# Kernel tuning notes

Measured on AMD Instinct MI355X. Metric: run time of the kernel, lower is better.

The kernel has to match this reference:

```python
import jax, jax.numpy as jnp
import numpy as np

TOP_K = 2


def setup_inputs() -> dict:
    key = jax.random.key(0)
    k1, k2, k3, k4, k5 = jax.random.split(key, 5)
    H, F, E = 1024, 2048, 8
    B, S = 2, 1024
    return {
        "hidden_states": jax.random.normal(k1, (B, S, H), dtype=jnp.float32),
        "gate_w": jax.random.normal(k2, (E, H), dtype=jnp.float32) * (1.0 / np.sqrt(H)),
        "w1": jax.random.normal(k3, (E, F, H), dtype=jnp.float32) * (1.0 / np.sqrt(H)),
        "w2": jax.random.normal(k4, (E, H, F), dtype=jnp.float32) * (1.0 / np.sqrt(F)),
        "w3": jax.random.normal(k5, (E, F, H), dtype=jnp.float32) * (1.0 / np.sqrt(H)),
    }


def reference(hidden_states, gate_w, w1, w2, w3):
    B, S, H = hidden_states.shape
    E = gate_w.shape[0]
    x = hidden_states.reshape(-1, H)  # [T, H]

    # Router: softmax in float32, top-k, renormalize (exact Mixtral math)
    router_logits = x @ gate_w.T  # [T, E]
    probs = jax.nn.softmax(router_logits.astype(jnp.float32), axis=-1)
    routing_weights, selected = jax.lax.top_k(probs, TOP_K)  # [T, K]
    routing_weights = routing_weights / routing_weights.sum(axis=-1, keepdims=True)
    routing_weights = routing_weights.astype(x.dtype)

    # Per-token combine weight for each expert: [T, E]
    combine = (jax.nn.one_hot(selected, E, dtype=x.dtype) * routing_weights[..., None]).sum(axis=1)

    # Dense grouped expert SwiGLU MLP (zero combine weight for unselected experts
    # makes this strictly equivalent to the gathered/dispatched computation)
    h = jnp.einsum('th,efh->etf', x, w1)   # [E, T, F]
    g = jnp.einsum('th,efh->etf', x, w3)   # [E, T, F]
    mid = jax.nn.silu(h) * g               # SwiGLU
    expert_out = jnp.einsum('etf,ehf->eth', mid, w2)  # [E, T, H]
    out = jnp.einsum('eth,te->th', expert_out, combine)  # weighted combine

    return out.reshape(B, S, H), router_logits
```

## Files before the change

### kernel.cpp

```cpp
#include <hip/hip_runtime.h>
#include <hip/hip_bf16.h>
#include <math.h>

#define H 1024
#define FF 2048
#define E 8
#define T 2048
#define NSLOT (2*T)
#define SLOT_PAD 128

typedef __attribute__((ext_vector_type(8))) short s16x8;
typedef __attribute__((ext_vector_type(4))) float f32x4;

static __device__ __forceinline__ unsigned short f2bf(float f) {
    union { float f; unsigned u; } v; v.f = f;
    unsigned r = v.u + 0x7fff + ((v.u >> 16) & 1);
    return (unsigned short)(r >> 16);
}

__global__ __launch_bounds__(256) void router_kernel(
    const float* __restrict__ x, const float* __restrict__ gw,
    float* __restrict__ logits_out, int* __restrict__ top_id,
    float* __restrict__ top_w, int* __restrict__ counts)
{
    int t = blockIdx.x;
    int tid = threadIdx.x;
    int e = tid >> 5;
    int l32 = tid & 31;
    const float* xr = x + (size_t)t * H;
    const float* gr = gw + (size_t)e * H;
    float s = 0.f;
    for (int h = l32; h < H; h += 32) s += xr[h] * gr[h];
    for (int off = 16; off; off >>= 1) s += __shfl_down(s, off, 32);
    __shared__ float lg[E];
    if (l32 == 0) lg[e] = s;
    __syncthreads();
    if (tid < E) logits_out[(size_t)t * E + tid] = lg[tid];
    if (tid == 0) {
        int i1 = 0; float b1 = lg[0];
        for (int i = 1; i < E; ++i) if (lg[i] > b1) { b1 = lg[i]; i1 = i; }
        int i2 = -1; float b2 = -INFINITY;
        for (int i = 0; i < E; ++i) if (i != i1 && lg[i] > b2) { b2 = lg[i]; i2 = i; }
        float p2 = expf(b2 - b1);
        float inv = 1.f / (1.f + p2);
        top_id[2*t]   = i1;  top_id[2*t+1] = i2;
        top_w[2*t]    = inv; top_w[2*t+1]  = p2 * inv;
        atomicAdd(&counts[i1], 1);
        atomicAdd(&counts[i2], 1);
    }
}

__global__ void scan_kernel(const int* __restrict__ counts,
                            int* __restrict__ offsets, int* __restrict__ cursors)
{
    if (threadIdx.x == 0) {
        int acc = 0;
        for (int i = 0; i < E; ++i) { offsets[i] = acc; acc += counts[i]; }
        offsets[E] = acc;
    }
    if (threadIdx.x < E) cursors[threadIdx.x] = 0;
}

__global__ __launch_bounds__(256) void assign_kernel(
    const float* __restrict__ x, const int* __restrict__ top_id,
    const float* __restrict__ top_w, const int* __restrict__ offsets,
    int* __restrict__ cursors, int* __restrict__ slot_token,
    float* __restrict__ slot_w, unsigned short* __restrict__ xg)
{
    int t = blockIdx.x, tid = threadIdx.x;
    __shared__ int pos[2];
    if (tid == 0) {
        for (int k = 0; k < 2; ++k) {
            int e = top_id[2*t + k];
            int p = offsets[e] + atomicAdd(&cursors[e], 1);
            slot_token[p] = t;
            slot_w[p] = top_w[2*t + k];
            pos[k] = p;
        }
    }
    __syncthreads();
    float4 xv = ((const float4*)(x + (size_t)t * H))[tid];
    ushort4 b;
    b.x = f2bf(xv.x); b.y = f2bf(xv.y); b.z = f2bf(xv.z); b.w = f2bf(xv.w);
    ((ushort4*)(xg + (size_t)pos[0] * H))[tid] = b;
    ((ushort4*)(xg + (size_t)pos[1] * H))[tid] = b;
}

__global__ __launch_bounds__(256) void gemm1_kernel(
    const unsigned short* __restrict__ xg,
    const float* __restrict__ w1, const float* __restrict__ w3,
    const int* __restrict__ offsets, unsigned short* __restrict__ mid)
{
    int e = blockIdx.z;
    int off = offsets[e];
    int cnt = offsets[e + 1] - off;
    int m0 = blockIdx.y * 128;
    if (m0 >= cnt) return;
    int f0 = blockIdx.x * 64;

    __shared__ __align__(16) unsigned short sx[128][72];
    __shared__ __align__(16) unsigned short s1[64][72];
    __shared__ __align__(16) unsigned short s3[64][72];

    int tid = threadIdx.x;
    int wave = tid >> 6, lane = tid & 63;
    int quad = lane >> 4, l16 = lane & 15;
    int wm = wave & 1, wn = wave >> 1;

    f32x4 acc1[4][2] = {{{0.f,0.f,0.f,0.f}}};
    f32x4 acc3[4][2] = {{{0.f,0.f,0.f,0.f}}};

    int sxr = tid >> 3, sxc = (tid & 7) * 8;
    int swr = tid >> 2, swc = (tid & 3) * 16;

    const unsigned short* xgp = xg + (size_t)(off + m0 + sxr) * H + sxc;
    const float* w1p = w1 + ((size_t)e * FF + f0 + swr) * H + swc;
    const float* w3p = w3 + ((size_t)e * FF + f0 + swr) * H + swc;

    for (int k0 = 0; k0 < H; k0 += 64) {
        #pragma unroll
        for (int rr = 0; rr < 128; rr += 32) {
            uint4 v = *(const uint4*)(xgp + (size_t)rr * H + k0);
            *(uint4*)&sx[sxr + rr][sxc] = v;
        }
        #pragma unroll
        for (int c = 0; c < 16; c += 4) {
            float4 a1 = *(const float4*)(w1p + k0 + c);
            float4 a3 = *(const float4*)(w3p + k0 + c);
            ushort4 c1, c3;
            c1.x = f2bf(a1.x); c1.y = f2bf(a1.y); c1.z = f2bf(a1.z); c1.w = f2bf(a1.w);
            c3.x = f2bf(a3.x); c3.y = f2bf(a3.y); c3.z = f2bf(a3.z); c3.w = f2bf(a3.w);
            *(ushort4*)&s1[swr][swc + c] = c1;
            *(ushort4*)&s3[swr][swc + c] = c3;
        }
        __syncthreads();
        #pragma unroll
        for (int ks = 0; ks < 2; ++ks) {
            int kk = ks * 32 + quad * 8;
            s16x8 a[4], b1[2], b3[2];
            #pragma unroll
            for (int i = 0; i < 4; ++i)
                a[i] = *(const s16x8*)&sx[wm * 64 + i * 16 + l16][kk];
            #pragma unroll
            for (int j = 0; j < 2; ++j) {
                b1[j] = *(const s16x8*)&s1[wn * 32 + j * 16 + l16][kk];
                b3[j] = *(const s16x8*)&s3[wn * 32 + j * 16 + l16][kk];
            }
            #pragma unroll
            for (int i = 0; i < 4; ++i)
                #pragma unroll
                for (int j = 0; j < 2; ++j) {
                    acc1[i][j] = __builtin_amdgcn_mfma_f32_16x16x32_bf16(a[i], b1[j], acc1[i][j], 0, 0, 0);
                    acc3[i][j] = __builtin_amdgcn_mfma_f32_16x16x32_bf16(a[i], b3[j], acc3[i][j], 0, 0, 0);
                }
        }
        __syncthreads();
    }

    #pragma unroll
    for (int i = 0; i < 4; ++i) {
        #pragma unroll
        for (int r = 0; r < 4; ++r) {
            int row = wm * 64 + i * 16 + quad * 4 + r;
            if (m0 + row < cnt) {
                size_t base = (size_t)(off + m0 + row) * FF + f0 + wn * 32;
                #pragma unroll
                for (int j = 0; j < 2; ++j) {
                    float h = acc1[i][j][r];
                    float g = acc3[i][j][r];
                    float v = h / (1.f + __expf(-h)) * g;
                    mid[base + j * 16 + l16] = f2bf(v);
                }
            }
        }
    }
}

__global__ __launch_bounds__(256) void gemm2_kernel(
    const unsigned short* __restrict__ mid, const float* __restrict__ w2,
    const int* __restrict__ offsets, const int* __restrict__ slot_token,
    const float* __restrict__ slot_w, float* __restrict__ out)
{
    int e = blockIdx.z;
    int off = offsets[e];
    int cnt = offsets[e + 1] - off;
    int m0 = blockIdx.y * 128;
    if (m0 >= cnt) return;
    int n0 = blockIdx.x * 64;

    __shared__ __align__(16) unsigned short sa[128][72];
    __shared__ __align__(16) unsigned short sb[64][72];

    int tid = threadIdx.x;
    int wave = tid >> 6, lane = tid & 63;
    int quad = lane >> 4, l16 = lane & 15;
    int wm = wave & 1, wn = wave >> 1;

    f32x4 acc[4][2] = {{{0.f,0.f,0.f,0.f}}};

    int sxr = tid >> 3, sxc = (tid & 7) * 8;
    int swr = tid >> 2, swc = (tid & 3) * 16;

    const unsigned short* ap = mid + (size_t)(off + m0 + sxr) * FF + sxc;
    const float* bp = w2 + ((size_t)e * H + n0 + swr) * FF + swc;

    for (int k0 = 0; k0 < FF; k0 += 64) {
        #pragma unroll
        for (int rr = 0; rr < 128; rr += 32) {
            uint4 v = *(const uint4*)(ap + (size_t)rr * FF + k0);
            *(uint4*)&sa[sxr + rr][sxc] = v;
        }
        #pragma unroll
        for (int c = 0; c < 16; c += 4) {
            float4 a = *(const float4*)(bp + k0 + c);
            ushort4 cb;
            cb.x = f2bf(a.x); cb.y = f2bf(a.y); cb.z = f2bf(a.z); cb.w = f2bf(a.w);
            *(ushort4*)&sb[swr][swc + c] = cb;
        }
        __syncthreads();
        #pragma unroll
        for (int ks = 0; ks < 2; ++ks) {
            int kk = ks * 32 + quad * 8;
            s16x8 a[4], b[2];
            #pragma unroll
            for (int i = 0; i < 4; ++i)
                a[i] = *(const s16x8*)&sa[wm * 64 + i * 16 + l16][kk];
            #pragma unroll
            for (int j = 0; j < 2; ++j)
                b[j] = *(const s16x8*)&sb[wn * 32 + j * 16 + l16][kk];
            #pragma unroll
            for (int i = 0; i < 4; ++i)
                #pragma unroll
                for (int j = 0; j < 2; ++j)
                    acc[i][j] = __builtin_amdgcn_mfma_f32_16x16x32_bf16(a[i], b[j], acc[i][j], 0, 0, 0);
        }
        __syncthreads();
    }

    #pragma unroll
    for (int i = 0; i < 4; ++i) {
        #pragma unroll
        for (int r = 0; r < 4; ++r) {
            int row = wm * 64 + i * 16 + quad * 4 + r;
            if (m0 + row < cnt) {
                int slot = off + m0 + row;
                int tok = slot_token[slot];
                float wgt = slot_w[slot];
                float* orow = out + (size_t)tok * H + n0 + wn * 32;
                #pragma unroll
                for (int j = 0; j < 2; ++j)
                    atomicAdd(&orow[j * 16 + l16], acc[i][j][r] * wgt);
            }
        }
    }
}

extern "C" void kernel_launch(void* const* d_in, const int* in_sizes, int n_in,
                              void* d_out, int out_size, void* d_ws, size_t ws_size,
                              hipStream_t stream) {
    const float* x  = (const float*)d_in[0];
    const float* gw = (const float*)d_in[1];
    const float* w1 = (const float*)d_in[2];
    const float* w2 = (const float*)d_in[3];
    const float* w3 = (const float*)d_in[4];
    float* out    = (float*)d_out;
    float* logits = out + (size_t)T * H;

    int* counts       = (int*)d_ws;
    int* cursors      = counts + 8;
    int* offsets      = cursors + 8;
    int* top_id       = counts + 64;
    float* top_w      = (float*)(top_id + 2*T);
    int* slot_token   = (int*)(top_w + 2*T);
    float* slot_w     = (float*)(slot_token + NSLOT);
    unsigned short* xg  = (unsigned short*)(slot_w + NSLOT);
    unsigned short* mid = xg + (size_t)(NSLOT + SLOT_PAD) * H;

    hipMemsetAsync(counts, 0, 64 * sizeof(int), stream);
    hipMemsetAsync(out, 0, (size_t)T * H * sizeof(float), stream);

    router_kernel<<<T, 256, 0, stream>>>(x, gw, logits, top_id, top_w, counts);
    scan_kernel<<<1, 64, 0, stream>>>(counts, offsets, cursors);
    assign_kernel<<<T, 256, 0, stream>>>(x, top_id, top_w, offsets, cursors,
                                         slot_token, slot_w, xg);
    gemm1_kernel<<<dim3(FF / 64, 16, E), 256, 0, stream>>>(xg, w1, w3, offsets, mid);
    gemm2_kernel<<<dim3(H / 64, 16, E), 256, 0, stream>>>(mid, w2, offsets,
                                                          slot_token, slot_w, out);
}
```

Baseline: 462.5 us.

## Pre-convert expert weights to bf16, use direct global-to-LDS loads, replace atomics with combine

```diff
diff --git a/kernel.cpp b/kernel.cpp
--- a/kernel.cpp
+++ b/kernel.cpp
@@ -16,6 +16,36 @@
     union { float f; unsigned u; } v; v.f = f;
     unsigned r = v.u + 0x7fff + ((v.u >> 16) & 1);
     return (unsigned short)(r >> 16);
+}
+static __device__ __forceinline__ float bf2f(unsigned short s) {
+    union { unsigned u; float f; } v; v.u = ((unsigned)s) << 16;
+    return v.f;
+}
+
+typedef __attribute__((address_space(3))) unsigned int lds_uint;
+typedef const __attribute__((address_space(1))) unsigned int glob_uint;
+static __device__ __forceinline__ void gl_lds16(const void* g, void* l) {
+    __builtin_amdgcn_global_load_lds((glob_uint*)g, (lds_uint*)l, 16, 0, 0);
+}
+
+__global__ __launch_bounds__(256) void convert_kernel(
+    const float* __restrict__ w1, const float* __restrict__ w3,
+    const float* __restrict__ w2, unsigned short* __restrict__ w1b,
+    unsigned short* __restrict__ w3b, unsigned short* __restrict__ w2b)
+{
+    const float* s; unsigned short* d;
+    if (blockIdx.y == 0)      { s = w1; d = w1b; }
+    else if (blockIdx.y == 1) { s = w3; d = w3b; }
+    else                      { s = w2; d = w2b; }
+    size_t i = ((size_t)blockIdx.x * 256 + threadIdx.x) * 8;
+    float4 a = *(const float4*)(s + i);
+    float4 b = *(const float4*)(s + i + 4);
+    uint4 st;
+    st.x = f2bf(a.x) | ((unsigned)f2bf(a.y) << 16);
+    st.y = f2bf(a.z) | ((unsigned)f2bf(a.w) << 16);
+    st.z = f2bf(b.x) | ((unsigned)f2bf(b.y) << 16);
+    st.w = f2bf(b.z) | ((unsigned)f2bf(b.w) << 16);
+    *(uint4*)(d + i) = st;
 }
 
 __global__ __launch_bounds__(256) void router_kernel(
@@ -63,9 +93,8 @@
 
 __global__ __launch_bounds__(256) void assign_kernel(
     const float* __restrict__ x, const int* __restrict__ top_id,
-    const float* __restrict__ top_w, const int* __restrict__ offsets,
-    int* __restrict__ cursors, int* __restrict__ slot_token,
-    float* __restrict__ slot_w, unsigned short* __restrict__ xg)
+    const int* __restrict__ offsets, int* __restrict__ cursors,
+    int* __restrict__ top_pos, unsigned short* __restrict__ xg)
 {
     int t = blockIdx.x, tid = threadIdx.x;
     __shared__ int pos[2];
@@ -73,8 +102,7 @@
         for (int k = 0; k < 2; ++k) {
             int e = top_id[2*t + k];
             int p = offsets[e] + atomicAdd(&cursors[e], 1);
-            slot_token[p] = t;
-            slot_w[p] = top_w[2*t + k];
+            top_pos[2*t + k] = p;
             pos[k] = p;
         }
     }
@@ -88,7 +116,7 @@
 
 __global__ __launch_bounds__(256) void gemm1_kernel(
     const unsigned short* __restrict__ xg,
-    const float* __restrict__ w1, const float* __restrict__ w3,
+    const unsigned short* __restrict__ w1b, const unsigned short* __restrict__ w3b,
     const int* __restrict__ offsets, unsigned short* __restrict__ mid)
 {
     int e = blockIdx.z;
@@ -98,60 +126,68 @@
     if (m0 >= cnt) return;
     int f0 = blockIdx.x * 64;
 
-    __shared__ __align__(16) unsigned short sx[128][72];
-    __shared__ __align__(16) unsigned short s1[64][72];
-    __shared__ __align__(16) unsigned short s3[64][72];
+    __shared__ __align__(16) unsigned short sx[128 * 64];
+    __shared__ __align__(16) unsigned short s1[64 * 64];
+    __shared__ __align__(16) unsigned short s3[64 * 64];
 
     int tid = threadIdx.x;
-    int wave = tid >> 6, lane = tid & 63;
-    int quad = lane >> 4, l16 = lane & 15;
-    int wm = wave & 1, wn = wave >> 1;
-
-    f32x4 acc1[4][2] = {{{0.f,0.f,0.f,0.f}}};
-    f32x4 acc3[4][2] = {{{0.f,0.f,0.f,0.f}}};
-
-    int sxr = tid >> 3, sxc = (tid & 7) * 8;
-    int swr = tid >> 2, swc = (tid & 3) * 16;
-
-    const unsigned short* xgp = xg + (size_t)(off + m0 + sxr) * H + sxc;
-    const float* w1p = w1 + ((size_t)e * FF + f0 + swr) * H + swc;
-    const float* w3p = w3 + ((size_t)e * FF + f0 + swr) * H + swc;
+    int wv = tid >> 6, ln = tid & 63;
+    int quad = ln >> 4, l16 = ln & 15;
+    int wm = wv & 1, wn = wv >> 1;
+    int xor7 = l16 & 7;
+
+    const unsigned short* xsrc[4]; unsigned short* xdst[4];
+    #pragma unroll
+    for (int j = 0; j < 4; ++j) {
+        int row = wv * 32 + j * 8 + (ln >> 3);
+        int cl = (ln & 7) ^ (row & 7);
+        xsrc[j] = xg + (size_t)(off + m0 + row) * H + cl * 8;
+        xdst[j] = &sx[(wv * 32 + j * 8) * 64];
+    }
+    const unsigned short *w1s[2], *w3s[2]; unsigned short *d1[2], *d3[2];
+    #pragma unroll
+    for (int j = 0; j < 2; ++j) {
+        int row = wv * 16 + j * 8 + (ln >> 3);
+        int cl = (ln & 7) ^ (row & 7);
+        w1s[j] = w1b + ((size_t)e * FF + f0 + row) * H + cl * 8;
+        w3s[j] = w3b + ((size_t)e * FF + f0 + row) * H + cl * 8;
+        d1[j] = &s1[(wv * 16 + j * 8) * 64];
+        d3[j] = &s3[(wv * 16 + j * 8) * 64];
+    }
+
+    f32x4 acc1[4][2], acc3[4][2];
+    #pragma unroll
+    for (int i = 0; i < 4; ++i)
+        #pragma unroll
+        for (int j = 0; j < 2; ++j) {
+            acc1[i][j] = (f32x4){0.f, 0.f, 0.f, 0.f};
+            acc3[i][j] = (f32x4){0.f, 0.f, 0.f, 0.f};
+        }
 
     for (int k0 = 0; k0 < H; k0 += 64) {
         #pragma unroll
-        for (int rr = 0; rr < 128; rr += 32) {
-            uint4 v = *(const uint4*)(xgp + (size_t)rr * H + k0);
-            *(uint4*)&sx[sxr + rr][sxc] = v;
-        }
-        #pragma unroll
-        for (int c = 0; c < 16; c += 4) {
-            float4 a1 = *(const float4*)(w1p + k0 + c);
-            float4 a3 = *(const float4*)(w3p + k0 + c);
-            ushort4 c1, c3;
-            c1.x = f2bf(a1.x); c1.y = f2bf(a1.y); c1.z = f2bf(a1.z); c1.w = f2bf(a1.w);
-            c3.x = f2bf(a3.x); c3.y = f2bf(a3.y); c3.z = f2bf(a3.z); c3.w = f2bf(a3.w);
-            *(ushort4*)&s1[swr][swc + c] = c1;
-            *(ushort4*)&s3[swr][swc + c] = c3;
-        }
+        for (int j = 0; j < 4; ++j) gl_lds16(xsrc[j] + k0, xdst[j]);
+        #pragma unroll
+        for (int j = 0; j < 2; ++j) { gl_lds16(w1s[j] + k0, d1[j]); gl_lds16(w3s[j] + k0, d3[j]); }
         __syncthreads();
         #pragma unroll
         for (int ks = 0; ks < 2; ++ks) {
-            int kk = ks * 32 + quad * 8;
-            s16x8 a[4], b1[2], b3[2];
+            int cph = ((quad + 4 * ks) ^ xor7) << 3;
+            s16x8 a[4], b1v[2], b3v[2];
             #pragma unroll
             for (int i = 0; i < 4; ++i)
-                a[i] = *(const s16x8*)&sx[wm * 64 + i * 16 + l16][kk];
+                a[i] = *(const s16x8*)&sx[(wm * 64 + i * 16 + l16) * 64 + cph];
             #pragma unroll
             for (int j = 0; j < 2; ++j) {
-                b1[j] = *(const s16x8*)&s1[wn * 32 + j * 16 + l16][kk];
-                b3[j] = *(const s16x8*)&s3[wn * 32 + j * 16 + l16][kk];
+                b1v[j] = *(const s16x8*)&s1[(wn * 32 + j * 16 + l16) * 64 + cph];
+                b3v[j] = *(const s16x8*)&s3[(wn * 32 + j * 16 + l16) * 64 + cph];
             }
             #pragma unroll
             for (int i = 0; i < 4; ++i)
                 #pragma unroll
                 for (int j = 0; j < 2; ++j) {
-                    acc1[i][j] = __builtin_amdgcn_mfma_f32_16x16x32_bf16(a[i], b1[j], acc1[i][j], 0, 0, 0);
-                    acc3[i][j] = __builtin_amdgcn_mfma_f32_16x16x32_bf16(a[i], b3[j], acc3[i][j], 0, 0, 0);
+                    acc1[i][j] = __builtin_amdgcn_mfma_f32_16x16x32_bf16(a[i], b1v[j], acc1[i][j], 0, 0, 0);
+                    acc3[i][j] = __builtin_amdgcn_mfma_f32_16x16x32_bf16(a[i], b3v[j], acc3[i][j], 0, 0, 0);
                 }
         }
         __syncthreads();
@@ -177,9 +213,8 @@
 }
 
 __global__ __launch_bounds__(256) void gemm2_kernel(
-    const unsigned short* __restrict__ mid, const float* __restrict__ w2,
-    const int* __restrict__ offsets, const int* __restrict__ slot_token,
-    const float* __restrict__ slot_w, float* __restrict__ out)
+    const unsigned short* __restrict__ mid, const unsigned short* __restrict__ w2b,
+    const int* __restrict__ offsets, unsigned short* __restrict__ y)
 {
     int e = blockIdx.z;
     int off = offsets[e];
@@ -188,46 +223,54 @@
     if (m0 >= cnt) return;
     int n0 = blockIdx.x * 64;
 
-    __shared__ __align__(16) unsigned short sa[128][72];
-    __shared__ __align__(16) unsigned short sb[64][72];
+    __shared__ __align__(16) unsigned short sa[128 * 64];
+    __shared__ __align__(16) unsigned short sb[64 * 64];
 
     int tid = threadIdx.x;
-    int wave = tid >> 6, lane = tid & 63;
-    int quad = lane >> 4, l16 = lane & 15;
-    int wm = wave & 1, wn = wave >> 1;
-
-    f32x4 acc[4][2] = {{{0.f,0.f,0.f,0.f}}};
-
-    int sxr = tid >> 3, sxc = (tid & 7) * 8;
-    int swr = tid >> 2, swc = (tid & 3) * 16;
-
-    const unsigned short* ap = mid + (size_t)(off + m0 + sxr) * FF + sxc;
-    const float* bp = w2 + ((size_t)e * H + n0 + swr) * FF + swc;
+    int wv = tid >> 6, ln = tid & 63;
+    int quad = ln >> 4, l16 = ln & 15;
+    int wm = wv & 1, wn = wv >> 1;
+    int xor7 = l16 & 7;
+
+    const unsigned short* asrc[4]; unsigned short* adst[4];
+    #pragma unroll
+    for (int j = 0; j < 4; ++j) {
+        int row = wv * 32 + j * 8 + (ln >> 3);
+        int cl = (ln & 7) ^ (row & 7);
+        asrc[j] = mid + (size_t)(off + m0 + row) * FF + cl * 8;
+        adst[j] = &sa[(wv * 32 + j * 8) * 64];
+    }
+    const unsigned short* bsrc[2]; unsigned short* bdst[2];
+    #pragma unroll
+    for (int j = 0; j < 2; ++j) {
+        int row = wv * 16 + j * 8 + (ln >> 3);
+        int cl = (ln & 7) ^ (row & 7);
+        bsrc[j] = w2b + ((size_t)e * H + n0 + row) * FF + cl * 8;
+        bdst[j] = &sb[(wv * 16 + j * 8) * 64];
+    }
+
+    f32x4 acc[4][2];
+    #pragma unroll
+    for (int i = 0; i < 4; ++i)
+        #pragma unroll
+        for (int j = 0; j < 2; ++j) acc[i][j] = (f32x4){0.f, 0.f, 0.f, 0.f};
 
     for (int k0 = 0; k0 < FF; k0 += 64) {
         #pragma unroll
-        for (int rr = 0; rr < 128; rr += 32) {
-            uint4 v = *(const uint4*)(ap + (size_t)rr * FF + k0);
-            *(uint4*)&sa[sxr + rr][sxc] = v;
-        }
-        #pragma unroll
-        for (int c = 0; c < 16; c += 4) {
-            float4 a = *(const float4*)(bp + k0 + c);
-            ushort4 cb;
-            cb.x = f2bf(a.x); cb.y = f2bf(a.y); cb.z = f2bf(a.z); cb.w = f2bf(a.w);
-            *(ushort4*)&sb[swr][swc + c] = cb;
-        }
+        for (int j = 0; j < 4; ++j) gl_lds16(asrc[j] + k0, adst[j]);
+        #pragma unroll
+        for (int j = 0; j < 2; ++j) gl_lds16(bsrc[j] + k0, bdst[j]);
         __syncthreads();
         #pragma unroll
         for (int ks = 0; ks < 2; ++ks) {
-            int kk = ks * 32 + quad * 8;
+            int cph = ((quad + 4 * ks) ^ xor7) << 3;
             s16x8 a[4], b[2];
             #pragma unroll
             for (int i = 0; i < 4; ++i)
-                a[i] = *(const s16x8*)&sa[wm * 64 + i * 16 + l16][kk];
+                a[i] = *(const s16x8*)&sa[(wm * 64 + i * 16 + l16) * 64 + cph];
             #pragma unroll
             for (int j = 0; j < 2; ++j)
-                b[j] = *(const s16x8*)&sb[wn * 32 + j * 16 + l16][kk];
+                b[j] = *(const s16x8*)&sb[(wn * 32 + j * 16 + l16) * 64 + cph];
             #pragma unroll
             for (int i = 0; i < 4; ++i)
                 #pragma unroll
@@ -243,16 +286,30 @@
         for (int r = 0; r < 4; ++r) {
             int row = wm * 64 + i * 16 + quad * 4 + r;
             if (m0 + row < cnt) {
-                int slot = off + m0 + row;
-                int tok = slot_token[slot];
-                float wgt = slot_w[slot];
-                float* orow = out + (size_t)tok * H + n0 + wn * 32;
+                size_t base = (size_t)(off + m0 + row) * H + n0 + wn * 32;
                 #pragma unroll
                 for (int j = 0; j < 2; ++j)
-                    atomicAdd(&orow[j * 16 + l16], acc[i][j][r] * wgt);
+                    y[base + j * 16 + l16] = f2bf(acc[i][j][r]);
             }
         }
     }
+}
+
+__global__ __launch_bounds__(256) void combine_kernel(
+    const unsigned short* __restrict__ y, const int* __restrict__ top_pos,
+    const float* __restrict__ top_w, float* __restrict__ out)
+{
+    int t = blockIdx.x, tid = threadIdx.x;
+    int p0 = top_pos[2*t], p1 = top_pos[2*t+1];
+    float w0 = top_w[2*t], w1 = top_w[2*t+1];
+    ushort4 a = ((const ushort4*)(y + (size_t)p0 * H))[tid];
+    ushort4 b = ((const ushort4*)(y + (size_t)p1 * H))[tid];
+    float4 o;
+    o.x = w0 * bf2f(a.x) + w1 * bf2f(b.x);
+    o.y = w0 * bf2f(a.y) + w1 * bf2f(b.y);
+    o.z = w0 * bf2f(a.z) + w1 * bf2f(b.z);
+    o.w = w0 * bf2f(a.w) + w1 * bf2f(b.w);
+    ((float4*)(out + (size_t)t * H))[tid] = o;
 }
 
 extern "C" void kernel_launch(void* const* d_in, const int* in_sizes, int n_in,
@@ -266,24 +323,26 @@
     float* out    = (float*)d_out;
     float* logits = out + (size_t)T * H;
 
-    int* counts       = (int*)d_ws;
-    int* cursors      = counts + 8;
-    int* offsets      = cursors + 8;
-    int* top_id       = counts + 64;
-    float* top_w      = (float*)(top_id + 2*T);
-    int* slot_token   = (int*)(top_w + 2*T);
-    float* slot_w     = (float*)(slot_token + NSLOT);
-    unsigned short* xg  = (unsigned short*)(slot_w + NSLOT);
-    unsigned short* mid = xg + (size_t)(NSLOT + SLOT_PAD) * H;
-
-    hipMemsetAsync(counts, 0, 64 * sizeof(int), stream);
-    hipMemsetAsync(out, 0, (size_t)T * H * sizeof(float), stream);
-
+    int* counts   = (int*)d_ws;
+    int* cursors  = counts + 8;
+    int* offsets  = counts + 16;
+    int* top_id   = counts + 32;
+    int* top_pos  = top_id + 2*T;
+    float* top_w  = (float*)(top_pos + 2*T);
+    unsigned short* xg  = (unsigned short*)(top_w + 2*T);
+    unsigned short* mid = xg  + (size_t)(NSLOT + SLOT_PAD) * H;
+    unsigned short* y   = mid + (size_t)(NSLOT + SLOT_PAD) * FF;
+    unsigned short* w1b = y   + (size_t)NSLOT * H;
+    unsigned short* w3b = w1b + (size_t)E * FF * H;
+    unsigned short* w2b = w3b + (size_t)E * FF * H;
+
+    hipMemsetAsync(counts, 0, 16 * sizeof(int), stream);
+
+    convert_kernel<<<dim3((E*FF*H)/(256*8), 3), 256, 0, stream>>>(w1, w3, w2, w1b, w3b, w2b);
     router_kernel<<<T, 256, 0, stream>>>(x, gw, logits, top_id, top_w, counts);
     scan_kernel<<<1, 64, 0, stream>>>(counts, offsets, cursors);
-    assign_kernel<<<T, 256, 0, stream>>>(x, top_id, top_w, offsets, cursors,
-                                         slot_token, slot_w, xg);
-    gemm1_kernel<<<dim3(FF / 64, 16, E), 256, 0, stream>>>(xg, w1, w3, offsets, mid);
-    gemm2_kernel<<<dim3(H / 64, 16, E), 256, 0, stream>>>(mid, w2, offsets,
-                                                          slot_token, slot_w, out);
-}
+    assign_kernel<<<T, 256, 0, stream>>>(x, top_id, offsets, cursors, top_pos, xg);
+    gemm1_kernel<<<dim3(FF / 64, 16, E), 256, 0, stream>>>(xg, w1b, w3b, offsets, mid);
+    gemm2_kernel<<<dim3(H / 64, 16, E), 256, 0, stream>>>(mid, w2b, offsets, y);
+    combine_kernel<<<T, 256, 0, stream>>>(y, top_pos, top_w, out);
+}
```

Measured after the change: 426.3 us. -7.8%, faster.
